# Optimization experiments

Measured on AMD Instinct MI355X. Metric: run time of the kernel, lower is better.

Reference implementation:

```python
import jax, jax.numpy as jnp
import numpy as np

NEG_W = 0.5  # negative_weight

def setup_inputs() -> dict:
    key = jax.random.key(0)
    ks = jax.random.split(key, 11)
    U, V, P, F, D, NF = 16384, 50000, 65536, 20, 64, 100000
    return {
        "user_emb": jax.random.normal(ks[0], (NF, D), jnp.float32),
        "item_emb": jax.random.normal(ks[1], (NF, D), jnp.float32),
        "w_user": jax.random.normal(ks[2], (NF,), jnp.float32),
        "w_item": jax.random.normal(ks[3], (NF,), jnp.float32),
        "bias": jax.random.normal(ks[4], (1,), jnp.float32),
        "h1": jax.random.normal(ks[5], (D,), jnp.float32),
        "h2": jax.random.normal(ks[6], (D,), jnp.float32),
        "user_feat_idx": jax.random.randint(ks[7], (U, F), 0, NF, jnp.int32),
        "item_feat_idx": jax.random.randint(ks[8], (V, F), 0, NF, jnp.int32),
        "pos_user_ids": jax.random.randint(ks[9], (P,), 0, U, jnp.int32),
        "pos_item_ids": jax.random.randint(ks[10], (P,), 0, V, jnp.int32),
    }

def _entity_terms(emb, w, feat_idx, h1, extra):
    # emb: [NF,D], feat_idx: [N,F] -> batched gather + FM bi-interaction
    g = emb[feat_idx]                      # [N,F,D]
    s = g.sum(axis=1)                      # [N,D]  (p_ud / q_vd)
    bi = 0.5 * (jnp.square(s) - jnp.square(g).sum(axis=1))  # [N,D]
    scalar = bi @ h1 + w[feat_idx].sum(axis=1) + extra       # [N]
    return s, scalar

def reference(user_emb, item_emb, w_user, w_item, bias, h1, h2,
              user_feat_idx, item_feat_idx, pos_user_ids, pos_item_ids):
    U = user_feat_idx.shape[0]
    V = item_feat_idx.shape[0]
    ones_u = jnp.ones((U, 1), user_emb.dtype)
    ones_v = jnp.ones((V, 1), item_emb.dtype)

    p_ud, su = _entity_terms(user_emb, w_user, user_feat_idx, h1, bias[0])
    q_vd, sv = _entity_terms(item_emb, w_item, item_feat_idx, h1, 0.0)
    p_u = jnp.concatenate([p_ud, su[:, None], ones_u], axis=1)  # [U,D+2]
    q_v = jnp.concatenate([q_vd, ones_v, sv[:, None]], axis=1)  # [V,D+2]

    # negative (all-pairs) term via D x D Gram matrices
    A = p_ud.T @ p_ud                                           # [D,D]
    B = q_vd.T @ q_vd                                           # [D,D]
    loss_neg = NEG_W * jnp.einsum('i,j,ij,ij->', h2, h2, A, B)

    # positive-pair term
    hv = jnp.concatenate([h2, jnp.ones((2,), h2.dtype)])        # [D+2]
    y = jnp.einsum('pd,pd,d->p', p_u[pos_user_ids], q_v[pos_item_ids], hv)
    loss_pos = jnp.sum((1.0 - NEG_W) * jnp.square(y) - 2.0 * y)

    return jnp.reshape(loss_neg + loss_pos, (1,))
```

## Files before the change

kernel.cpp:

```cpp
#include <hip/hip_runtime.h>

#define FD 20
#define DD 64

#define GA 64
#define GB 128
#define GAB 16
#define GBB 32
#define POSB 2048
#define NEGB 64

typedef float float2v __attribute__((ext_vector_type(2)));
typedef float float4v __attribute__((ext_vector_type(4)));
typedef unsigned short ushort4v __attribute__((ext_vector_type(4)));
typedef unsigned short ushort8v __attribute__((ext_vector_type(8)));
typedef short short8v __attribute__((ext_vector_type(8)));

__device__ __forceinline__ unsigned short f2bf(float f) {
    unsigned u = __float_as_uint(f);
    unsigned r = u + 0x7fffu + ((u >> 16) & 1u);
    return (unsigned short)(r >> 16);
}
__device__ __forceinline__ float bf2f(unsigned short h) {
    return __uint_as_float((unsigned)h << 16);
}

__global__ __launch_bounds__(256) void conv_kernel(
    const float* __restrict__ ue, const float* __restrict__ ie,
    unsigned int* __restrict__ u8, unsigned int* __restrict__ i8,
    int n4, float* __restrict__ out, int out_size)
{
    int i = blockIdx.x * blockDim.x + threadIdx.x;
    if (i < out_size) out[i] = 0.0f;
    if (i >= 2 * n4) return;
    const float4v* src; unsigned int* dst; int k;
    if (i < n4) { src = (const float4v*)ue; dst = u8; k = i; }
    else        { src = (const float4v*)ie; dst = i8; k = i - n4; }
    float4v v = src[k];
    unsigned int p = 0;
    p = __builtin_amdgcn_cvt_pk_fp8_f32(v.x, v.y, p, false);
    p = __builtin_amdgcn_cvt_pk_fp8_f32(v.z, v.w, p, true);
    dst[k] = p;
}

__global__ __launch_bounds__(256, 4) void entity_kernel(
    const unsigned char* __restrict__ user_f8,
    const unsigned char* __restrict__ item_f8,
    const float* __restrict__ w_user, const float* __restrict__ w_item,
    const float* __restrict__ bias, const float* __restrict__ h1,
    const int* __restrict__ ufeat, const int* __restrict__ ifeat,
    unsigned short* __restrict__ p_bf, float* __restrict__ su,
    unsigned short* __restrict__ q_bf, float* __restrict__ sv,
    int U, int V)
{
    int gwid = (int)((blockIdx.x * blockDim.x + threadIdx.x) >> 6);
    int lane = threadIdx.x & 63;
    int eg   = lane >> 4;
    int c    = lane & 15;
    int ent  = gwid * 4 + eg;
    if (ent >= U + V) return;

    bool isU = ent < U;
    int  m   = isU ? ent : ent - U;
    const unsigned char* emb = isU ? user_f8 : item_f8;
    const float* wv   = isU ? w_user : w_item;
    const int*   fidx = (isU ? ufeat : ifeat) + (size_t)m * FD;
    float extra       = isU ? bias[0] : 0.0f;
    unsigned short* srow = (isU ? p_bf : q_bf) + (size_t)m * DD;
    float* sc         = (isU ? su : sv) + m;

    int idx[FD];
#pragma unroll
    for (int j = 0; j < FD; ++j) idx[j] = fidx[j];

    unsigned int hw[FD];
#pragma unroll
    for (int j = 0; j < FD; ++j)
        hw[j] = *((const unsigned int*)(emb + (size_t)idx[j] * DD) + c);

    float4v s4 = (float4v)0.0f, ss4 = (float4v)0.0f;
#pragma unroll
    for (int j = 0; j < FD; ++j) {
        float2v lo = __builtin_amdgcn_cvt_pk_f32_fp8(hw[j], false);
        float2v hi = __builtin_amdgcn_cvt_pk_f32_fp8(hw[j], true);
        float4v g;
        g.x = lo.x; g.y = lo.y; g.z = hi.x; g.w = hi.y;
        s4 += g; ss4 += g * g;
    }

    float part = wv[idx[c]];
    if (c < FD - 16) part += wv[idx[16 + c]];

    float4v h14 = *(const float4v*)(h1 + c * 4);
    float4v bi4 = 0.5f * (s4 * s4 - ss4);
    part += bi4.x*h14.x + bi4.y*h14.y + bi4.z*h14.z + bi4.w*h14.w;

#pragma unroll
    for (int off = 1; off <= 8; off <<= 1)
        part += __shfl_xor(part, off, 64);

    ushort4v o;
    o.x = f2bf(s4.x); o.y = f2bf(s4.y); o.z = f2bf(s4.z); o.w = f2bf(s4.w);
    *(ushort4v*)(srow + c * 4) = o;

    if (c == 0) *sc = part + extra;
}

__device__ __forceinline__ void gram_block_mfma(
    const unsigned short* __restrict__ M, int nrows, int gwid, int nw,
    float* __restrict__ Gpart)
{
    int lane = threadIdx.x & 63;
    int q = lane >> 4;
    int c = lane & 15;

    float4v acc[4][4];
#pragma unroll
    for (int ti = 0; ti < 4; ++ti)
#pragma unroll
        for (int tj = 0; tj < 4; ++tj)
            acc[ti][tj] = (float4v)0.0f;

    int ntiles = (nrows + 63) >> 6;
    for (int tt = gwid; tt < ntiles; tt += nw) {
        int row0 = tt << 6;
#pragma unroll
        for (int kb = 0; kb < 2; ++kb) {
            int r0 = row0 + kb * 32 + q * 8;
            const unsigned short* base = M + (size_t)r0 * DD + c;
            short8v f[4];
            if (row0 + 64 <= nrows) {
#pragma unroll
                for (int Db = 0; Db < 4; ++Db)
#pragma unroll
                    for (int j = 0; j < 8; ++j)
                        f[Db][j] = (short)base[(size_t)j * DD + Db * 16];
            } else {
#pragma unroll
                for (int Db = 0; Db < 4; ++Db)
#pragma unroll
                    for (int j = 0; j < 8; ++j)
                        f[Db][j] = (r0 + j < nrows)
                                 ? (short)base[(size_t)j * DD + Db * 16]
                                 : (short)0;
            }
#pragma unroll
            for (int ti = 0; ti < 4; ++ti)
#pragma unroll
                for (int tj = 0; tj < 4; ++tj)
                    acc[ti][tj] = __builtin_amdgcn_mfma_f32_16x16x32_bf16(
                        f[ti], f[tj], acc[ti][tj], 0, 0, 0);
        }
    }

    float* out = Gpart + (size_t)gwid * (DD * DD);
#pragma unroll
    for (int ti = 0; ti < 4; ++ti)
#pragma unroll
        for (int tj = 0; tj < 4; ++tj)
#pragma unroll
            for (int rg = 0; rg < 4; ++rg)
                out[(ti * 16 + q * 4 + rg) * DD + tj * 16 + c] = acc[ti][tj][rg];
}

__global__ __launch_bounds__(256) void mid_kernel(
    const unsigned short* __restrict__ p_bf, int U, float* __restrict__ PA,
    const unsigned short* __restrict__ q_bf, int V, float* __restrict__ PB,
    const float* __restrict__ su, const float* __restrict__ sv,
    const float* __restrict__ h2,
    const int* __restrict__ pu, const int* __restrict__ pi,
    int P, float* __restrict__ posPart)
{
    __shared__ float red[4];
    int w = threadIdx.x >> 6;

    if (blockIdx.x < GAB) {
        gram_block_mfma(p_bf, U, blockIdx.x * 4 + w, GA, PA);
        return;
    }
    if (blockIdx.x < GAB + GBB) {
        gram_block_mfma(q_bf, V, (blockIdx.x - GAB) * 4 + w, GB, PB);
        return;
    }

    int lane = threadIdx.x & 63;
    int sl   = lane & 15;
    int sub  = lane >> 4;
    int pb   = blockIdx.x - (GAB + GBB);
    int wId  = pb * 4 + w;
    const int NW = POSB * 4;

    float4v h2v = *(const float4v*)(h2 + sl * 4);

    int pid0 = wId * 4 + sub;
    int pid1 = pid0 + NW * 4;
    bool ok0 = pid0 < P, ok1 = pid1 < P;

    int u0 = 0, v0 = 0, u1 = 0, v1 = 0;
    if (ok0) { u0 = pu[pid0]; v0 = pi[pid0]; }
    if (ok1) { u1 = pu[pid1]; v1 = pi[pid1]; }

    ushort4v ph0 = (ushort4v)0, qh0 = (ushort4v)0;
    ushort4v ph1 = (ushort4v)0, qh1 = (ushort4v)0;
    if (ok0) {
        ph0 = *(const ushort4v*)(p_bf + (size_t)u0 * DD + sl * 4);
        qh0 = *(const ushort4v*)(q_bf + (size_t)v0 * DD + sl * 4);
    }
    if (ok1) {
        ph1 = *(const ushort4v*)(p_bf + (size_t)u1 * DD + sl * 4);
        qh1 = *(const ushort4v*)(q_bf + (size_t)v1 * DD + sl * 4);
    }

    float d0 = bf2f(ph0.x)*bf2f(qh0.x)*h2v.x + bf2f(ph0.y)*bf2f(qh0.y)*h2v.y
             + bf2f(ph0.z)*bf2f(qh0.z)*h2v.z + bf2f(ph0.w)*bf2f(qh0.w)*h2v.w;
    float d1 = bf2f(ph1.x)*bf2f(qh1.x)*h2v.x + bf2f(ph1.y)*bf2f(qh1.y)*h2v.y
             + bf2f(ph1.z)*bf2f(qh1.z)*h2v.z + bf2f(ph1.w)*bf2f(qh1.w)*h2v.w;
#pragma unroll
    for (int off = 1; off < 16; off <<= 1) {
        d0 += __shfl_xor(d0, off, 64);
        d1 += __shfl_xor(d1, off, 64);
    }

    float acc = 0.0f;
    if (sl == 0) {
        if (ok0) { float y = d0 + su[u0] + sv[v0]; acc += 0.5f * y * y - 2.0f * y; }
        if (ok1) { float y = d1 + su[u1] + sv[v1]; acc += 0.5f * y * y - 2.0f * y; }
    }
    acc += __shfl_xor(acc, 16, 64);
    acc += __shfl_xor(acc, 32, 64);
    if (lane == 0) red[w] = acc;
    __syncthreads();
    if (threadIdx.x == 0)
        posPart[pb] = red[0] + red[1] + red[2] + red[3];
}

__global__ __launch_bounds__(256) void neg_reduce_kernel(
    const float* __restrict__ PA, const float* __restrict__ PB,
    const float* __restrict__ h2, const float* __restrict__ posPart,
    float* __restrict__ out)
{
    __shared__ float sA[4][64], sB[4][64];
    __shared__ float sPos;
    int t  = threadIdx.x;
    int l  = t & 63;
    int ch = t >> 6;
    int e  = blockIdx.x * 64 + l;

    float a = 0.0f, b = 0.0f;
#pragma unroll
    for (int k = 0; k < GA / 4; ++k)
        a += PA[(size_t)(ch * (GA / 4) + k) * (DD * DD) + e];
#pragma unroll
    for (int k = 0; k < GB / 4; ++k)
        b += PB[(size_t)(ch * (GB / 4) + k) * (DD * DD) + e];
    sA[ch][l] = a;
    sB[ch][l] = b;

    if (ch == 1) {
        float p = (l < POSB / NEGB) ? posPart[blockIdx.x * (POSB / NEGB) + l] : 0.0f;
#pragma unroll
        for (int off = 1; off <= 32; off <<= 1)
            p += __shfl_xor(p, off, 64);
        if (l == 0) sPos = p;
    }
    __syncthreads();

    if (ch == 0) {
        float fa = sA[0][l] + sA[1][l] + sA[2][l] + sA[3][l];
        float fb = sB[0][l] + sB[1][l] + sB[2][l] + sB[3][l];
        float acc = 0.5f * h2[blockIdx.x] * h2[l] * fa * fb;
#pragma unroll
        for (int off = 1; off <= 32; off <<= 1)
            acc += __shfl_xor(acc, off, 64);
        if (l == 0)
            atomicAdd(out, acc + sPos);
    }
}

extern "C" void kernel_launch(void* const* d_in, const int* in_sizes, int n_in,
                              void* d_out, int out_size, void* d_ws, size_t ws_size,
                              hipStream_t stream)
{
    const float* user_emb = (const float*)d_in[0];
    const float* item_emb = (const float*)d_in[1];
    const float* w_user   = (const float*)d_in[2];
    const float* w_item   = (const float*)d_in[3];
    const float* bias     = (const float*)d_in[4];
    const float* h1       = (const float*)d_in[5];
    const float* h2       = (const float*)d_in[6];
    const int*   ufeat    = (const int*)d_in[7];
    const int*   ifeat    = (const int*)d_in[8];
    const int*   pu       = (const int*)d_in[9];
    const int*   pi       = (const int*)d_in[10];

    const int NF = in_sizes[0] / DD;
    const int U  = in_sizes[7] / FD;
    const int V  = in_sizes[8] / FD;
    const int P  = in_sizes[9];

    float* ws = (float*)d_ws;
    size_t off = 0;
    unsigned short* p_bf = (unsigned short*)(ws + off); off += (size_t)U * DD / 2;
    unsigned short* q_bf = (unsigned short*)(ws + off); off += (size_t)V * DD / 2;
    float* su   = ws + off; off += (size_t)U;          off = (off + 63) & ~(size_t)63;
    float* sv   = ws + off; off += (size_t)V;          off = (off + 63) & ~(size_t)63;
    float* PA   = ws + off; off += (size_t)GA * DD * DD;
    float* PB   = ws + off; off += (size_t)GB * DD * DD;
    float* posPart = ws + off; off += (size_t)POSB;    off = (off + 63) & ~(size_t)63;
    unsigned char* uf8 = (unsigned char*)(ws + off);   off += (size_t)NF * DD / 4;
    unsigned char* if8 = (unsigned char*)(ws + off);   off += (size_t)NF * DD / 4;

    float* out = (float*)d_out;

    int n4 = NF * DD / 4;
    conv_kernel<<<(2 * n4 + 255) / 256, 256, 0, stream>>>(
        user_emb, item_emb, (unsigned int*)uf8, (unsigned int*)if8,
        n4, out, out_size);

    int nent = U + V;
    int nwaves = (nent + 3) / 4;
    entity_kernel<<<(nwaves + 3) / 4, 256, 0, stream>>>(
        uf8, if8, w_user, w_item, bias, h1,
        ufeat, ifeat, p_bf, su, q_bf, sv, U, V);

    mid_kernel<<<GAB + GBB + POSB, 256, 0, stream>>>(
        p_bf, U, PA, q_bf, V, PB, su, sv, h2, pu, pi, P, posPart);

    neg_reduce_kernel<<<NEGB, 256, 0, stream>>>(PA, PB, h2, posPart, out);
}
```

Before: 144.4 us.

## Fuse final reduction into mid kernel via last-blocks atomic counter

Drops the separate neg_reduce launch. Each mid_kernel block increments a global done counter, and the last NEGB blocks to arrive wait for the count to reach the total, then run the Gram and positive-part reduction. The counter is reset in conv_kernel. This removes one kernel launch and its gap, at the cost of spin-waiting blocks and extra fences in every block.

```diff
diff --git a/kernel.cpp b/kernel.cpp
--- a/kernel.cpp
+++ b/kernel.cpp
@@ -9,6 +9,7 @@
 #define GBB 32
 #define POSB 2048
 #define NEGB 64
+#define TOTALB (GAB + GBB + POSB)
 
 typedef float float2v __attribute__((ext_vector_type(2)));
 typedef float float4v __attribute__((ext_vector_type(4)));
@@ -28,10 +29,12 @@
 __global__ __launch_bounds__(256) void conv_kernel(
     const float* __restrict__ ue, const float* __restrict__ ie,
     unsigned int* __restrict__ u8, unsigned int* __restrict__ i8,
-    int n4, float* __restrict__ out, int out_size)
+    int n4, float* __restrict__ out, int out_size,
+    unsigned int* __restrict__ done)
 {
     int i = blockIdx.x * blockDim.x + threadIdx.x;
     if (i < out_size) out[i] = 0.0f;
+    if (i == 0) *done = 0u;
     if (i >= 2 * n4) return;
     const float4v* src; unsigned int* dst; int k;
     if (i < n4) { src = (const float4v*)ue; dst = u8; k = i; }
@@ -169,82 +172,92 @@
     const float* __restrict__ su, const float* __restrict__ sv,
     const float* __restrict__ h2,
     const int* __restrict__ pu, const int* __restrict__ pi,
-    int P, float* __restrict__ posPart)
+    int P, float* __restrict__ posPart,
+    unsigned int* __restrict__ done, float* __restrict__ out)
 {
     __shared__ float red[4];
+    __shared__ float sA[4][64], sB[4][64];
+    __shared__ float sPos;
+    __shared__ unsigned int s_old;
     int w = threadIdx.x >> 6;
+    int lane = threadIdx.x & 63;
 
     if (blockIdx.x < GAB) {
         gram_block_mfma(p_bf, U, blockIdx.x * 4 + w, GA, PA);
-        return;
-    }
-    if (blockIdx.x < GAB + GBB) {
+    } else if (blockIdx.x < GAB + GBB) {
         gram_block_mfma(q_bf, V, (blockIdx.x - GAB) * 4 + w, GB, PB);
-        return;
-    }
-
-    int lane = threadIdx.x & 63;
-    int sl   = lane & 15;
-    int sub  = lane >> 4;
-    int pb   = blockIdx.x - (GAB + GBB);
-    int wId  = pb * 4 + w;
-    const int NW = POSB * 4;
-
-    float4v h2v = *(const float4v*)(h2 + sl * 4);
-
-    int pid0 = wId * 4 + sub;
-    int pid1 = pid0 + NW * 4;
-    bool ok0 = pid0 < P, ok1 = pid1 < P;
-
-    int u0 = 0, v0 = 0, u1 = 0, v1 = 0;
-    if (ok0) { u0 = pu[pid0]; v0 = pi[pid0]; }
-    if (ok1) { u1 = pu[pid1]; v1 = pi[pid1]; }
-
-    ushort4v ph0 = (ushort4v)0, qh0 = (ushort4v)0;
-    ushort4v ph1 = (ushort4v)0, qh1 = (ushort4v)0;
-    if (ok0) {
-        ph0 = *(const ushort4v*)(p_bf + (size_t)u0 * DD + sl * 4);
-        qh0 = *(const ushort4v*)(q_bf + (size_t)v0 * DD + sl * 4);
-    }
-    if (ok1) {
-        ph1 = *(const ushort4v*)(p_bf + (size_t)u1 * DD + sl * 4);
-        qh1 = *(const ushort4v*)(q_bf + (size_t)v1 * DD + sl * 4);
-    }
-
-    float d0 = bf2f(ph0.x)*bf2f(qh0.x)*h2v.x + bf2f(ph0.y)*bf2f(qh0.y)*h2v.y
-             + bf2f(ph0.z)*bf2f(qh0.z)*h2v.z + bf2f(ph0.w)*bf2f(qh0.w)*h2v.w;
-    float d1 = bf2f(ph1.x)*bf2f(qh1.x)*h2v.x + bf2f(ph1.y)*bf2f(qh1.y)*h2v.y
-             + bf2f(ph1.z)*bf2f(qh1.z)*h2v.z + bf2f(ph1.w)*bf2f(qh1.w)*h2v.w;
-#pragma unroll
-    for (int off = 1; off < 16; off <<= 1) {
-        d0 += __shfl_xor(d0, off, 64);
-        d1 += __shfl_xor(d1, off, 64);
-    }
-
-    float acc = 0.0f;
-    if (sl == 0) {
-        if (ok0) { float y = d0 + su[u0] + sv[v0]; acc += 0.5f * y * y - 2.0f * y; }
-        if (ok1) { float y = d1 + su[u1] + sv[v1]; acc += 0.5f * y * y - 2.0f * y; }
-    }
-    acc += __shfl_xor(acc, 16, 64);
-    acc += __shfl_xor(acc, 32, 64);
-    if (lane == 0) red[w] = acc;
+    } else {
+        int sl   = lane & 15;
+        int sub  = lane >> 4;
+        int pb   = blockIdx.x - (GAB + GBB);
+        int wId  = pb * 4 + w;
+        const int NW = POSB * 4;
+
+        float4v h2v = *(const float4v*)(h2 + sl * 4);
+
+        int pid0 = wId * 4 + sub;
+        int pid1 = pid0 + NW * 4;
+        bool ok0 = pid0 < P, ok1 = pid1 < P;
+
+        int u0 = 0, v0 = 0, u1 = 0, v1 = 0;
+        if (ok0) { u0 = pu[pid0]; v0 = pi[pid0]; }
+        if (ok1) { u1 = pu[pid1]; v1 = pi[pid1]; }
+
+        ushort4v ph0 = (ushort4v)0, qh0 = (ushort4v)0;
+        ushort4v ph1 = (ushort4v)0, qh1 = (ushort4v)0;
+        if (ok0) {
+            ph0 = *(const ushort4v*)(p_bf + (size_t)u0 * DD + sl * 4);
+            qh0 = *(const ushort4v*)(q_bf + (size_t)v0 * DD + sl * 4);
+        }
+        if (ok1) {
+            ph1 = *(const ushort4v*)(p_bf + (size_t)u1 * DD + sl * 4);
+            qh1 = *(const ushort4v*)(q_bf + (size_t)v1 * DD + sl * 4);
+        }
+
+        float d0 = bf2f(ph0.x)*bf2f(qh0.x)*h2v.x + bf2f(ph0.y)*bf2f(qh0.y)*h2v.y
+                 + bf2f(ph0.z)*bf2f(qh0.z)*h2v.z + bf2f(ph0.w)*bf2f(qh0.w)*h2v.w;
+        float d1 = bf2f(ph1.x)*bf2f(qh1.x)*h2v.x + bf2f(ph1.y)*bf2f(qh1.y)*h2v.y
+                 + bf2f(ph1.z)*bf2f(qh1.z)*h2v.z + bf2f(ph1.w)*bf2f(qh1.w)*h2v.w;
+#pragma unroll
+        for (int off = 1; off < 16; off <<= 1) {
+            d0 += __shfl_xor(d0, off, 64);
+            d1 += __shfl_xor(d1, off, 64);
+        }
+
+        float acc = 0.0f;
+        if (sl == 0) {
+            if (ok0) { float y = d0 + su[u0] + sv[v0]; acc += 0.5f * y * y - 2.0f * y; }
+            if (ok1) { float y = d1 + su[u1] + sv[v1]; acc += 0.5f * y * y - 2.0f * y; }
+        }
+        acc += __shfl_xor(acc, 16, 64);
+        acc += __shfl_xor(acc, 32, 64);
+        if (lane == 0) red[w] = acc;
+        __syncthreads();
+        if (threadIdx.x == 0)
+            posPart[pb] = red[0] + red[1] + red[2] + red[3];
+    }
+
+    __threadfence();
     __syncthreads();
     if (threadIdx.x == 0)
-        posPart[pb] = red[0] + red[1] + red[2] + red[3];
-}
-
-__global__ __launch_bounds__(256) void neg_reduce_kernel(
-    const float* __restrict__ PA, const float* __restrict__ PB,
-    const float* __restrict__ h2, const float* __restrict__ posPart,
-    float* __restrict__ out)
-{
-    __shared__ float sA[4][64], sB[4][64];
-    __shared__ float sPos;
+        s_old = atomicAdd(done, 1u);
+    __syncthreads();
+    unsigned int old = s_old;
+    if (old < (unsigned)(TOTALB - NEGB)) return;
+    int rid = (int)(old - (unsigned)(TOTALB - NEGB));
+
+    if (threadIdx.x == 0) {
+        while (__hip_atomic_load(done, __ATOMIC_RELAXED,
+                                 __HIP_MEMORY_SCOPE_AGENT) < (unsigned)TOTALB)
+            __builtin_amdgcn_s_sleep(2);
+    }
+    __syncthreads();
+    __threadfence();
+
     int t  = threadIdx.x;
     int l  = t & 63;
     int ch = t >> 6;
-    int e  = blockIdx.x * 64 + l;
+    int e  = rid * 64 + l;
 
     float a = 0.0f, b = 0.0f;
 #pragma unroll
@@ -257,7 +270,7 @@
     sB[ch][l] = b;
 
     if (ch == 1) {
-        float p = (l < POSB / NEGB) ? posPart[blockIdx.x * (POSB / NEGB) + l] : 0.0f;
+        float p = (l < POSB / NEGB) ? posPart[rid * (POSB / NEGB) + l] : 0.0f;
 #pragma unroll
         for (int off = 1; off <= 32; off <<= 1)
             p += __shfl_xor(p, off, 64);
@@ -268,7 +281,7 @@
     if (ch == 0) {
         float fa = sA[0][l] + sA[1][l] + sA[2][l] + sA[3][l];
         float fb = sB[0][l] + sB[1][l] + sB[2][l] + sB[3][l];
-        float acc = 0.5f * h2[blockIdx.x] * h2[l] * fa * fb;
+        float acc = 0.5f * h2[rid] * h2[l] * fa * fb;
 #pragma unroll
         for (int off = 1; off <= 32; off <<= 1)
             acc += __shfl_xor(acc, off, 64);
@@ -307,6 +320,7 @@
     float* PA   = ws + off; off += (size_t)GA * DD * DD;
     float* PB   = ws + off; off += (size_t)GB * DD * DD;
     float* posPart = ws + off; off += (size_t)POSB;    off = (off + 63) & ~(size_t)63;
+    unsigned int* done = (unsigned int*)(ws + off);    off += 16;
     unsigned char* uf8 = (unsigned char*)(ws + off);   off += (size_t)NF * DD / 4;
     unsigned char* if8 = (unsigned char*)(ws + off);   off += (size_t)NF * DD / 4;
 
@@ -315,7 +329,7 @@
     int n4 = NF * DD / 4;
     conv_kernel<<<(2 * n4 + 255) / 256, 256, 0, stream>>>(
         user_emb, item_emb, (unsigned int*)uf8, (unsigned int*)if8,
-        n4, out, out_size);
+        n4, out, out_size, done);
 
     int nent = U + V;
     int nwaves = (nent + 3) / 4;
@@ -323,8 +337,7 @@
         uf8, if8, w_user, w_item, bias, h1,
         ufeat, ifeat, p_bf, su, q_bf, sv, U, V);
 
-    mid_kernel<<<GAB + GBB + POSB, 256, 0, stream>>>(
-        p_bf, U, PA, q_bf, V, PB, su, sv, h2, pu, pi, P, posPart);
-
-    neg_reduce_kernel<<<NEGB, 256, 0, stream>>>(PA, PB, h2, posPart, out);
-}
+    mid_kernel<<<TOTALB, 256, 0, stream>>>(
+        p_bf, U, PA, q_bf, V, PB, su, sv, h2, pu, pi, P, posPart,
+        done, out);
+}
```

Result: slower. 320.3 us (+121.8%).
